# Performance work log

Hardware: AMD Instinct MI355X
Metric: run time of the kernel (lower is better)

The kernel has to match this reference:

```python
import jax, jax.numpy as jnp
import numpy as np

B = 512          # batch
D = 2048         # num_variables / leaf folds of a balanced binary region graph
K = 32           # num_units (sum/input units per fold)


def setup_inputs() -> dict:
    key = jax.random.key(0)
    k1, k2, k3 = jax.random.split(key, 3)
    # input-layer log-densities per (variable-region, unit): [B, D, K]
    x = jax.random.normal(k1, (B, D, K), dtype=jnp.float32)
    # packed per-fold CP mixing weights for all inner layers: sum_l F_l = D-1 folds
    weights = jax.random.uniform(k2, (D - 1, K, K), dtype=jnp.float32,
                                 minval=0.01, maxval=1.0)  # positive (monotonic)
    # packed fold_idx bookkeeping: layer l gathers children (2f, 2f+1) of prev layer
    idx_list = []
    F = D
    while F > 1:
        F //= 2
        idx_list.append(np.arange(2 * F, dtype=np.int32).reshape(F, 2))
    fold_idx = jnp.asarray(np.concatenate(idx_list, axis=0))  # [D-1, 2]
    # out-mixture logits over the root's K units (num_classes = 1)
    mix_logw = jax.random.normal(k3, (K,), dtype=jnp.float32)
    return {"x": x, "weights": weights, "fold_idx": fold_idx, "mix_logw": mix_logw}


def _log_matmul_exp(a, w):
    # a: [B, F, K] log-values; w: [F, K, Kout] positive weights
    # y_j = log sum_i exp(a_i) * w_ij, computed stably via max-subtraction
    m = jnp.max(a, axis=-1, keepdims=True)
    y = jnp.einsum('bfi,fij->bfj', jnp.exp(a - m), w)
    return jnp.log(y) + m


def reference(x, weights, fold_idx, mix_logw):
    # DAG evaluation: gather via fold_idx, CP layer = log-product of the two
    # gathered children followed by a per-fold log-linear mixture.
    out = x                      # [B, F, K]
    off = 0
    F = x.shape[1]
    while F > 1:                 # static Python loop over log2(D)=11 layers
        F //= 2
        idx = fold_idx[off:off + F]            # [F, 2] child indices (static slice)
        inp = out[:, idx, :]                   # gather -> [B, F, 2, K]
        prod = inp[:, :, 0, :] + inp[:, :, 1, :]   # log-space product node
        out = _log_matmul_exp(prod, weights[off:off + F])  # sum node -> [B, F, K]
        off += F
    # Born real path: outputs = 2 * real(log amp), then MonotonicMixtureLayer
    flat = 2.0 * out[:, 0, :]                  # [B, K]
    logw = jax.nn.log_softmax(mix_logw)        # normalized mixture weights
    return jax.nn.logsumexp(flat + logw[None, :], axis=-1)  # [B]
```

## Files before the change

kernel.cpp:

```cpp
#include <hip/hip_runtime.h>

#define KK 32
#define BATCH 512
#define DD 2048
#define ESTRIDE 36
#define NUNIT (KK * BATCH)

__device__ __forceinline__ float max8(const float p[8]) {
  const float a0 = fmaxf(p[0], p[1]), a1 = fmaxf(p[2], p[3]);
  const float a2 = fmaxf(p[4], p[5]), a3 = fmaxf(p[6], p[7]);
  return fmaxf(fmaxf(a0, a1), fmaxf(a2, a3));
}
__device__ __forceinline__ float max4pm(const float* pm, int lane) {
  return fmaxf(fmaxf(pm[lane], pm[65 + lane]),
               fmaxf(pm[130 + lane], pm[195 + lane]));
}
__device__ __forceinline__ void write_e(float* __restrict__ E, int lane,
                                        int j0, const float p[8], float m) {
  float4* ew = reinterpret_cast<float4*>(E + lane * ESTRIDE + j0);
  ew[0] = make_float4(__expf(p[0] - m), __expf(p[1] - m), __expf(p[2] - m),
                      __expf(p[3] - m));
  ew[1] = make_float4(__expf(p[4] - m), __expf(p[5] - m), __expf(p[6] - m),
                      __expf(p[7] - m));
}
__device__ __forceinline__ void addv8(const float a[8], const float b[8],
                                      float o[8]) {
#pragma unroll
  for (int j = 0; j < 8; ++j) o[j] = a[j] + b[j];
}

#define MAC8(acc, e, w0, w1)                                   \
  acc[0] = fmaf(e, w0.x, acc[0]); acc[1] = fmaf(e, w0.y, acc[1]); \
  acc[2] = fmaf(e, w0.z, acc[2]); acc[3] = fmaf(e, w0.w, acc[3]); \
  acc[4] = fmaf(e, w1.x, acc[4]); acc[5] = fmaf(e, w1.y, acc[5]); \
  acc[6] = fmaf(e, w1.z, acc[6]); acc[7] = fmaf(e, w1.w, acc[7]);

__device__ __forceinline__ void node8_pair(
    const float pa[8], const float pb[8], const float* __restrict__ Wa,
    const float* __restrict__ Wb, float* __restrict__ Ea,
    float* __restrict__ Eb, float* __restrict__ pm, int jg, int lane, int j0,
    float oa[8], float ob[8]) {
  pm[jg * 65 + lane] = max8(pa);
  pm[260 + jg * 65 + lane] = max8(pb);
  __syncthreads();
  const float ma = max4pm(pm, lane);
  const float mb = max4pm(pm + 260, lane);
  write_e(Ea, lane, j0, pa, ma);
  write_e(Eb, lane, j0, pb, mb);
  __syncthreads();

  const float4* era = reinterpret_cast<const float4*>(Ea + lane * ESTRIDE);
  const float4* erb = reinterpret_cast<const float4*>(Eb + lane * ESTRIDE);
  const float4* WLa = reinterpret_cast<const float4*>(Wa) + (j0 >> 2);
  const float4* WLb = reinterpret_cast<const float4*>(Wb) + (j0 >> 2);

  float acca[8], accb[8];
#pragma unroll
  for (int j = 0; j < 8; ++j) { acca[j] = 0.0f; accb[j] = 0.0f; }

#pragma unroll 1
  for (int q = 0; q < 8; ++q) {
    const float4 eva = era[q];
    const float4 evb = erb[q];
    const int i0 = 4 * q;
    {
      const float4 w0 = WLa[(i0 + 0) * 8], w1 = WLa[(i0 + 0) * 8 + 1];
      const float4 v0 = WLb[(i0 + 0) * 8], v1 = WLb[(i0 + 0) * 8 + 1];
      MAC8(acca, eva.x, w0, w1) MAC8(accb, evb.x, v0, v1)
    }
    {
      const float4 w0 = WLa[(i0 + 1) * 8], w1 = WLa[(i0 + 1) * 8 + 1];
      const float4 v0 = WLb[(i0 + 1) * 8], v1 = WLb[(i0 + 1) * 8 + 1];
      MAC8(acca, eva.y, w0, w1) MAC8(accb, evb.y, v0, v1)
    }
    {
      const float4 w0 = WLa[(i0 + 2) * 8], w1 = WLa[(i0 + 2) * 8 + 1];
      const float4 v0 = WLb[(i0 + 2) * 8], v1 = WLb[(i0 + 2) * 8 + 1];
      MAC8(acca, eva.z, w0, w1) MAC8(accb, evb.z, v0, v1)
    }
    {
      const float4 w0 = WLa[(i0 + 3) * 8], w1 = WLa[(i0 + 3) * 8 + 1];
      const float4 v0 = WLb[(i0 + 3) * 8], v1 = WLb[(i0 + 3) * 8 + 1];
      MAC8(acca, eva.w, w0, w1) MAC8(accb, evb.w, v0, v1)
    }
  }
#pragma unroll
  for (int j = 0; j < 8; ++j) {
    oa[j] = __logf(acca[j]) + ma;
    ob[j] = __logf(accb[j]) + mb;
  }
}

__device__ __forceinline__ void node8L(const float p8[8],
                                       const float* __restrict__ Wt,
                                       float* __restrict__ E,
                                       float* __restrict__ pm, int jg,
                                       int lane, int j0, float o8[8]) {
  pm[jg * 65 + lane] = max8(p8);
  __syncthreads();
  const float m = max4pm(pm, lane);
  write_e(E, lane, j0, p8, m);
  __syncthreads();

  const float4* er = reinterpret_cast<const float4*>(E + lane * ESTRIDE);
  const float4* WL = reinterpret_cast<const float4*>(Wt) + (j0 >> 2);
  float acc[8];
#pragma unroll
  for (int j = 0; j < 8; ++j) acc[j] = 0.0f;
#pragma unroll 1
  for (int q = 0; q < 8; ++q) {
    const float4 ev = er[q];
    const int i0 = 4 * q;
    const float4 wa0 = WL[(i0 + 0) * 8], wa1 = WL[(i0 + 0) * 8 + 1];
    const float4 wb0 = WL[(i0 + 1) * 8], wb1 = WL[(i0 + 1) * 8 + 1];
    const float4 wc0 = WL[(i0 + 2) * 8], wc1 = WL[(i0 + 2) * 8 + 1];
    const float4 wd0 = WL[(i0 + 3) * 8], wd1 = WL[(i0 + 3) * 8 + 1];
    MAC8(acc, ev.x, wa0, wa1) MAC8(acc, ev.y, wb0, wb1)
    MAC8(acc, ev.z, wc0, wc1) MAC8(acc, ev.w, wd0, wd1)
  }
#pragma unroll
  for (int j = 0; j < 8; ++j) o8[j] = __logf(acc[j]) + m;
}

__device__ __forceinline__ void pairload_x(const float* __restrict__ xb,
                                           int leaf, int j0, float p[8]) {
  const float4* u = reinterpret_cast<const float4*>(xb + leaf * KK + j0);
  const float4* v = reinterpret_cast<const float4*>(xb + (leaf + 1) * KK + j0);
  const float4 u0 = u[0], u1 = u[1], v0 = v[0], v1 = v[1];
  p[0] = u0.x + v0.x; p[1] = u0.y + v0.y; p[2] = u0.z + v0.z; p[3] = u0.w + v0.w;
  p[4] = u1.x + v1.x; p[5] = u1.y + v1.y; p[6] = u1.z + v1.z; p[7] = u1.w + v1.w;
}

__device__ __forceinline__ void pairload_n(const float* __restrict__ in,
                                           int node, int j0, int b, float p[8]) {
  const float* p0 = in + (size_t)node * NUNIT + (size_t)j0 * BATCH + b;
  const float* p1 = p0 + NUNIT;
#pragma unroll
  for (int k = 0; k < 8; ++k) p[k] = p0[k * BATCH] + p1[k * BATCH];
}

__global__ __launch_bounds__(256, 4) void kern1(const float* __restrict__ x,
                                                const float* __restrict__ W,
                                                float* __restrict__ o) {
  __shared__ __align__(16) float W_lds[7 * KK * KK];
  __shared__ __align__(16) float Ea[64 * ESTRIDE];
  __shared__ __align__(16) float Eb[64 * ESTRIDE];
  __shared__ float pm[2 * 260];
  const int tid = threadIdx.x;
  const int lane = tid & 63;
  const int jg = __builtin_amdgcn_readfirstlane(tid >> 6);
  const int j0 = jg * 8;
  const int b = blockIdx.y * 64 + lane;
  const int chunk = blockIdx.x;
  const int c4 = chunk * 4, c2 = chunk * 2;

  const float4* W4 = reinterpret_cast<const float4*>(W);
  float4* WL4 = reinterpret_cast<float4*>(W_lds);
  WL4[tid]        = W4[(size_t)(c4 + 0) * 256 + tid];
  WL4[256 + tid]  = W4[(size_t)(c4 + 1) * 256 + tid];
  WL4[512 + tid]  = W4[(size_t)(c4 + 2) * 256 + tid];
  WL4[768 + tid]  = W4[(size_t)(c4 + 3) * 256 + tid];
  WL4[1024 + tid] = W4[(size_t)(1024 + c2 + 0) * 256 + tid];
  WL4[1280 + tid] = W4[(size_t)(1024 + c2 + 1) * 256 + tid];
  WL4[1536 + tid] = W4[(size_t)(1536 + chunk) * 256 + tid];

  const float* xb = x + (size_t)b * (DD * KK) + (size_t)chunk * 8 * KK;
  float pA0[8], pB0[8], pA1[8], pB1[8];
  pairload_x(xb, 0, j0, pA0);
  pairload_x(xb, 2, j0, pB0);
  pairload_x(xb, 4, j0, pA1);
  pairload_x(xb, 6, j0, pB1);

  float n0[8], n1[8], n2[8], n3[8], m0[8], m1[8], o8[8], p[8], q[8];

  node8_pair(pA0, pB0, W_lds + 0 * 1024, W_lds + 1 * 1024, Ea, Eb, pm, jg,
             lane, j0, n0, n1);
  node8_pair(pA1, pB1, W_lds + 2 * 1024, W_lds + 3 * 1024, Ea, Eb, pm, jg,
             lane, j0, n2, n3);
  addv8(n0, n1, p);
  addv8(n2, n3, q);
  node8_pair(p, q, W_lds + 4 * 1024, W_lds + 5 * 1024, Ea, Eb, pm, jg, lane,
             j0, m0, m1);
  addv8(m0, m1, p);
  node8L(p, W_lds + 6 * 1024, Ea, pm, jg, lane, j0, o8);

#pragma unroll
  for (int j = 0; j < 8; ++j)
    o[(size_t)chunk * NUNIT + (size_t)(j0 + j) * BATCH + b] = o8[j];
}

__global__ __launch_bounds__(256, 4) void kernT(const float* __restrict__ in,
                                                const float* __restrict__ W,
                                                float* __restrict__ o, int lo,
                                                int hi) {
  __shared__ __align__(16) float W_lds[3 * KK * KK];
  __shared__ __align__(16) float Ea[64 * ESTRIDE];
  __shared__ __align__(16) float Eb[64 * ESTRIDE];
  __shared__ float pm[2 * 260];
  const int tid = threadIdx.x;
  const int lane = tid & 63;
  const int jg = __builtin_amdgcn_readfirstlane(tid >> 6);
  const int j0 = jg * 8;
  const int b = blockIdx.y * 64 + lane;
  const int n = blockIdx.x;

  const float4* W4 = reinterpret_cast<const float4*>(W);
  float4* WL4 = reinterpret_cast<float4*>(W_lds);
  WL4[tid]       = W4[(size_t)(lo + 2 * n + 0) * 256 + tid];
  WL4[256 + tid] = W4[(size_t)(lo + 2 * n + 1) * 256 + tid];
  WL4[512 + tid] = W4[(size_t)(hi + n) * 256 + tid];

  float pa[8], pb[8], r0[8], r1[8], p[8], o8[8];
  pairload_n(in, 4 * n + 0, j0, b, pa);
  pairload_n(in, 4 * n + 2, j0, b, pb);
  node8_pair(pa, pb, W_lds, W_lds + 1024, Ea, Eb, pm, jg, lane, j0, r0, r1);
  addv8(r0, r1, p);
  node8L(p, W_lds + 2048, Ea, pm, jg, lane, j0, o8);

#pragma unroll
  for (int j = 0; j < 8; ++j)
    o[(size_t)n * NUNIT + (size_t)(j0 + j) * BATCH + b] = o8[j];
}

__global__ __launch_bounds__(256, 4) void kernF(const float* __restrict__ in,
                                                const float* __restrict__ W,
                                                const float* __restrict__ mixw,
                                                float* __restrict__ out) {
  __shared__ __align__(16) float W_lds[3 * KK * KK];
  __shared__ __align__(16) float Ea[64 * ESTRIDE];
  __shared__ __align__(16) float Eb[64 * ESTRIDE];
  __shared__ float pm[2 * 260];
  const int tid = threadIdx.x;
  const int lane = tid & 63;
  const int jg = __builtin_amdgcn_readfirstlane(tid >> 6);
  const int j0 = jg * 8;
  const int b = blockIdx.y * 64 + lane;

  const float4* W4 = reinterpret_cast<const float4*>(W);
  float4* WL4 = reinterpret_cast<float4*>(W_lds);
  WL4[tid]       = W4[(size_t)2044 * 256 + tid];
  WL4[256 + tid] = W4[(size_t)2045 * 256 + tid];
  WL4[512 + tid] = W4[(size_t)2046 * 256 + tid];

  float pa[8], pb[8], r0[8], r1[8], p[8], o8[8];
  pairload_n(in, 0, j0, b, pa);
  pairload_n(in, 2, j0, b, pb);
  node8_pair(pa, pb, W_lds, W_lds + 1024, Ea, Eb, pm, jg, lane, j0, r0, r1);
  addv8(r0, r1, p);
  node8L(p, W_lds + 2048, Ea, pm, jg, lane, j0, o8);

  float wv32[KK];
#pragma unroll
  for (int i = 0; i < KK; ++i) wv32[i] = mixw[i];
  float t[KK];
#pragma unroll
  for (int i = 0; i < KK; ++i) t[i] = wv32[i];
#pragma unroll
  for (int s = KK / 2; s >= 1; s >>= 1)
#pragma unroll
    for (int i = 0; i < s; ++i) t[i] = fmaxf(t[i], t[i + s]);
  const float wm = t[0];
  float ws = 0.0f;
#pragma unroll
  for (int i = 0; i < KK; ++i) ws += __expf(wv32[i] - wm);
  const float lsew = __logf(ws) + wm;

  float t8[8];
#pragma unroll
  for (int j = 0; j < 8; ++j) t8[j] = 2.0f * o8[j] + (wv32[j0 + j] - lsew);
  __syncthreads();
  pm[jg * 65 + lane] = max8(t8);
  __syncthreads();
  const float m2 = max4pm(pm, lane);
  float ss = 0.0f;
#pragma unroll
  for (int j = 0; j < 8; ++j) ss += __expf(t8[j] - m2);
  __syncthreads();
  pm[jg * 65 + lane] = ss;
  __syncthreads();
  if (jg == 0) {
    const float s4 = (pm[lane] + pm[65 + lane]) + (pm[130 + lane] + pm[195 + lane]);
    out[b] = __logf(s4) + m2;
  }
}

extern "C" void kernel_launch(void* const* d_in, const int* in_sizes, int n_in,
                              void* d_out, int out_size, void* d_ws,
                              size_t ws_size, hipStream_t stream) {
  const float* x = (const float*)d_in[0];
  const float* W = (const float*)d_in[1];
  const float* mixw = (const float*)d_in[3];
  float* out = (float*)d_out;

  float* A = (float*)d_ws;
  float* Bb = A + (size_t)256 * NUNIT;

  kern1<<<dim3(256, 8), 256, 0, stream>>>(x, W, A);
  kernT<<<dim3(64, 8), 256, 0, stream>>>(A, W, Bb, 1792, 1920);
  kernT<<<dim3(16, 8), 256, 0, stream>>>(Bb, W, A, 1984, 2016);
  kernT<<<dim3(4, 8), 256, 0, stream>>>(A, W, Bb, 2032, 2040);
  kernF<<<dim3(1, 8), 256, 0, stream>>>(Bb, W, mixw, out);
}
```

Before: 244.0 us.

## Compute full 32-unit nodes per thread in registers, drop LDS and barriers

Each thread now owns one batch element and evaluates whole 32-wide nodes in registers. Weights are read directly from global memory at block-uniform addresses, so they can be served by scalar loads, and the LDS staging plus the cross-wave max reductions and their barriers are gone. Intermediate activations switch from a unit-major [node][unit][batch] layout to [node][batch][unit], so each thread reads and writes its own contiguous rows with float4 accesses. The trade-off is much higher register pressure (several 32-float arrays live at once) and four times fewer launched blocks, which lowers occupancy and leaves less room to hide latency.

```diff
diff --git a/kernel.cpp b/kernel.cpp
--- a/kernel.cpp
+++ b/kernel.cpp
@@ -3,285 +3,181 @@
 #define KK 32
 #define BATCH 512
 #define DD 2048
-#define ESTRIDE 36
-#define NUNIT (KK * BATCH)
+#define NODEF (BATCH * KK)
 
-__device__ __forceinline__ float max8(const float p[8]) {
-  const float a0 = fmaxf(p[0], p[1]), a1 = fmaxf(p[2], p[3]);
-  const float a2 = fmaxf(p[4], p[5]), a3 = fmaxf(p[6], p[7]);
-  return fmaxf(fmaxf(a0, a1), fmaxf(a2, a3));
-}
-__device__ __forceinline__ float max4pm(const float* pm, int lane) {
-  return fmaxf(fmaxf(pm[lane], pm[65 + lane]),
-               fmaxf(pm[130 + lane], pm[195 + lane]));
-}
-__device__ __forceinline__ void write_e(float* __restrict__ E, int lane,
-                                        int j0, const float p[8], float m) {
-  float4* ew = reinterpret_cast<float4*>(E + lane * ESTRIDE + j0);
-  ew[0] = make_float4(__expf(p[0] - m), __expf(p[1] - m), __expf(p[2] - m),
-                      __expf(p[3] - m));
-  ew[1] = make_float4(__expf(p[4] - m), __expf(p[5] - m), __expf(p[6] - m),
-                      __expf(p[7] - m));
-}
-__device__ __forceinline__ void addv8(const float a[8], const float b[8],
-                                      float o[8]) {
+__device__ __forceinline__ void node32(float p[KK], const float* __restrict__ Wn) {
+  float t[16];
 #pragma unroll
-  for (int j = 0; j < 8; ++j) o[j] = a[j] + b[j];
+  for (int i = 0; i < 16; ++i) t[i] = fmaxf(p[2 * i], p[2 * i + 1]);
+#pragma unroll
+  for (int s = 8; s >= 1; s >>= 1)
+#pragma unroll
+    for (int i = 0; i < s; ++i) t[i] = fmaxf(t[i], t[i + s]);
+  const float m = t[0];
+
+#pragma unroll
+  for (int i = 0; i < KK; ++i) p[i] = __expf(p[i] - m);
+
+  float acc[KK];
+#pragma unroll
+  for (int j = 0; j < KK; ++j) acc[j] = 0.0f;
+
+#pragma unroll 8
+  for (int i = 0; i < KK; ++i) {
+    const float ei = p[i];
+#pragma unroll
+    for (int j = 0; j < KK; ++j)
+      acc[j] = fmaf(ei, Wn[i * KK + j], acc[j]);
+  }
+
+#pragma unroll
+  for (int j = 0; j < KK; ++j) p[j] = __logf(acc[j]) + m;
 }
 
-#define MAC8(acc, e, w0, w1)                                   \
-  acc[0] = fmaf(e, w0.x, acc[0]); acc[1] = fmaf(e, w0.y, acc[1]); \
-  acc[2] = fmaf(e, w0.z, acc[2]); acc[3] = fmaf(e, w0.w, acc[3]); \
-  acc[4] = fmaf(e, w1.x, acc[4]); acc[5] = fmaf(e, w1.y, acc[5]); \
-  acc[6] = fmaf(e, w1.z, acc[6]); acc[7] = fmaf(e, w1.w, acc[7]);
-
-__device__ __forceinline__ void node8_pair(
-    const float pa[8], const float pb[8], const float* __restrict__ Wa,
-    const float* __restrict__ Wb, float* __restrict__ Ea,
-    float* __restrict__ Eb, float* __restrict__ pm, int jg, int lane, int j0,
-    float oa[8], float ob[8]) {
-  pm[jg * 65 + lane] = max8(pa);
-  pm[260 + jg * 65 + lane] = max8(pb);
-  __syncthreads();
-  const float ma = max4pm(pm, lane);
-  const float mb = max4pm(pm + 260, lane);
-  write_e(Ea, lane, j0, pa, ma);
-  write_e(Eb, lane, j0, pb, mb);
-  __syncthreads();
-
-  const float4* era = reinterpret_cast<const float4*>(Ea + lane * ESTRIDE);
-  const float4* erb = reinterpret_cast<const float4*>(Eb + lane * ESTRIDE);
-  const float4* WLa = reinterpret_cast<const float4*>(Wa) + (j0 >> 2);
-  const float4* WLb = reinterpret_cast<const float4*>(Wb) + (j0 >> 2);
-
-  float acca[8], accb[8];
+__device__ __forceinline__ void pairsum_g(const float* __restrict__ a,
+                                          const float* __restrict__ b,
+                                          float p[KK]) {
+  const float4* u = reinterpret_cast<const float4*>(a);
+  const float4* v = reinterpret_cast<const float4*>(b);
+  float4 ub[8], vb[8];
 #pragma unroll
-  for (int j = 0; j < 8; ++j) { acca[j] = 0.0f; accb[j] = 0.0f; }
-
-#pragma unroll 1
+  for (int q = 0; q < 8; ++q) ub[q] = u[q];
+#pragma unroll
+  for (int q = 0; q < 8; ++q) vb[q] = v[q];
+#pragma unroll
   for (int q = 0; q < 8; ++q) {
-    const float4 eva = era[q];
-    const float4 evb = erb[q];
-    const int i0 = 4 * q;
-    {
-      const float4 w0 = WLa[(i0 + 0) * 8], w1 = WLa[(i0 + 0) * 8 + 1];
-      const float4 v0 = WLb[(i0 + 0) * 8], v1 = WLb[(i0 + 0) * 8 + 1];
-      MAC8(acca, eva.x, w0, w1) MAC8(accb, evb.x, v0, v1)
-    }
-    {
-      const float4 w0 = WLa[(i0 + 1) * 8], w1 = WLa[(i0 + 1) * 8 + 1];
-      const float4 v0 = WLb[(i0 + 1) * 8], v1 = WLb[(i0 + 1) * 8 + 1];
-      MAC8(acca, eva.y, w0, w1) MAC8(accb, evb.y, v0, v1)
-    }
-    {
-      const float4 w0 = WLa[(i0 + 2) * 8], w1 = WLa[(i0 + 2) * 8 + 1];
-      const float4 v0 = WLb[(i0 + 2) * 8], v1 = WLb[(i0 + 2) * 8 + 1];
-      MAC8(acca, eva.z, w0, w1) MAC8(accb, evb.z, v0, v1)
-    }
-    {
-      const float4 w0 = WLa[(i0 + 3) * 8], w1 = WLa[(i0 + 3) * 8 + 1];
-      const float4 v0 = WLb[(i0 + 3) * 8], v1 = WLb[(i0 + 3) * 8 + 1];
-      MAC8(acca, eva.w, w0, w1) MAC8(accb, evb.w, v0, v1)
-    }
-  }
-#pragma unroll
-  for (int j = 0; j < 8; ++j) {
-    oa[j] = __logf(acca[j]) + ma;
-    ob[j] = __logf(accb[j]) + mb;
+    p[4 * q + 0] = ub[q].x + vb[q].x;
+    p[4 * q + 1] = ub[q].y + vb[q].y;
+    p[4 * q + 2] = ub[q].z + vb[q].z;
+    p[4 * q + 3] = ub[q].w + vb[q].w;
   }
 }
 
-__device__ __forceinline__ void node8L(const float p8[8],
-                                       const float* __restrict__ Wt,
-                                       float* __restrict__ E,
-                                       float* __restrict__ pm, int jg,
-                                       int lane, int j0, float o8[8]) {
-  pm[jg * 65 + lane] = max8(p8);
-  __syncthreads();
-  const float m = max4pm(pm, lane);
-  write_e(E, lane, j0, p8, m);
-  __syncthreads();
-
-  const float4* er = reinterpret_cast<const float4*>(E + lane * ESTRIDE);
-  const float4* WL = reinterpret_cast<const float4*>(Wt) + (j0 >> 2);
-  float acc[8];
+__device__ __forceinline__ void store32(float* __restrict__ dst, const float p[KK]) {
+  float4* d = reinterpret_cast<float4*>(dst);
 #pragma unroll
-  for (int j = 0; j < 8; ++j) acc[j] = 0.0f;
-#pragma unroll 1
-  for (int q = 0; q < 8; ++q) {
-    const float4 ev = er[q];
-    const int i0 = 4 * q;
-    const float4 wa0 = WL[(i0 + 0) * 8], wa1 = WL[(i0 + 0) * 8 + 1];
-    const float4 wb0 = WL[(i0 + 1) * 8], wb1 = WL[(i0 + 1) * 8 + 1];
-    const float4 wc0 = WL[(i0 + 2) * 8], wc1 = WL[(i0 + 2) * 8 + 1];
-    const float4 wd0 = WL[(i0 + 3) * 8], wd1 = WL[(i0 + 3) * 8 + 1];
-    MAC8(acc, ev.x, wa0, wa1) MAC8(acc, ev.y, wb0, wb1)
-    MAC8(acc, ev.z, wc0, wc1) MAC8(acc, ev.w, wd0, wd1)
-  }
-#pragma unroll
-  for (int j = 0; j < 8; ++j) o8[j] = __logf(acc[j]) + m;
+  for (int q = 0; q < 8; ++q)
+    d[q] = make_float4(p[4 * q], p[4 * q + 1], p[4 * q + 2], p[4 * q + 3]);
 }
 
-__device__ __forceinline__ void pairload_x(const float* __restrict__ xb,
-                                           int leaf, int j0, float p[8]) {
-  const float4* u = reinterpret_cast<const float4*>(xb + leaf * KK + j0);
-  const float4* v = reinterpret_cast<const float4*>(xb + (leaf + 1) * KK + j0);
-  const float4 u0 = u[0], u1 = u[1], v0 = v[0], v1 = v[1];
-  p[0] = u0.x + v0.x; p[1] = u0.y + v0.y; p[2] = u0.z + v0.z; p[3] = u0.w + v0.w;
-  p[4] = u1.x + v1.x; p[5] = u1.y + v1.y; p[6] = u1.z + v1.z; p[7] = u1.w + v1.w;
+__global__ __launch_bounds__(256) void kern1(const float* __restrict__ x,
+                                             const float* __restrict__ W,
+                                             float* __restrict__ o) {
+  const int tid = threadIdx.x;
+  const int lane = tid & 63;
+  const int wid = tid >> 6;
+  const int chunk = blockIdx.x;
+  const int b = blockIdx.y * 256 + wid * 64 + lane;
+
+  const float* xb = x + (size_t)b * (DD * KK) + (size_t)chunk * 8 * KK;
+  const float* WL1 = W + (size_t)(4 * chunk) * (KK * KK);
+  const float* WL2 = W + (size_t)(1024 + 2 * chunk) * (KK * KK);
+  const float* WL3 = W + (size_t)(1536 + chunk) * (KK * KK);
+
+  float s01[KK], s23[KK], p[KK];
+
+  pairsum_g(xb + 0 * KK, xb + 1 * KK, s01);
+  node32(s01, WL1 + 0 * 1024);
+  pairsum_g(xb + 2 * KK, xb + 3 * KK, p);
+  node32(p, WL1 + 1 * 1024);
+#pragma unroll
+  for (int j = 0; j < KK; ++j) s01[j] += p[j];
+
+  pairsum_g(xb + 4 * KK, xb + 5 * KK, s23);
+  node32(s23, WL1 + 2 * 1024);
+  pairsum_g(xb + 6 * KK, xb + 7 * KK, p);
+  node32(p, WL1 + 3 * 1024);
+#pragma unroll
+  for (int j = 0; j < KK; ++j) s23[j] += p[j];
+
+  node32(s01, WL2 + 0 * 1024);
+  node32(s23, WL2 + 1 * 1024);
+#pragma unroll
+  for (int j = 0; j < KK; ++j) s01[j] += s23[j];
+
+  node32(s01, WL3);
+
+  store32(o + ((size_t)chunk * BATCH + b) * KK, s01);
 }
 
-__device__ __forceinline__ void pairload_n(const float* __restrict__ in,
-                                           int node, int j0, int b, float p[8]) {
-  const float* p0 = in + (size_t)node * NUNIT + (size_t)j0 * BATCH + b;
-  const float* p1 = p0 + NUNIT;
+__global__ __launch_bounds__(256) void kernT(const float* __restrict__ in,
+                                             const float* __restrict__ W,
+                                             float* __restrict__ o, int lo,
+                                             int hi) {
+  const int tid = threadIdx.x;
+  const int lane = tid & 63;
+  const int wid = tid >> 6;
+  const int n = blockIdx.x;
+  const int b = blockIdx.y * 256 + wid * 64 + lane;
+
+  const float* i0 = in + ((size_t)(4 * n) * BATCH + b) * KK;
+
+  float s01[KK], p[KK];
+
+  pairsum_g(i0, i0 + NODEF, s01);
+  node32(s01, W + (size_t)(lo + 2 * n + 0) * (KK * KK));
+  pairsum_g(i0 + 2 * (size_t)NODEF, i0 + 3 * (size_t)NODEF, p);
+  node32(p, W + (size_t)(lo + 2 * n + 1) * (KK * KK));
 #pragma unroll
-  for (int k = 0; k < 8; ++k) p[k] = p0[k * BATCH] + p1[k * BATCH];
+  for (int j = 0; j < KK; ++j) s01[j] += p[j];
+
+  node32(s01, W + (size_t)(hi + n) * (KK * KK));
+
+  store32(o + ((size_t)n * BATCH + b) * KK, s01);
 }
 
-__global__ __launch_bounds__(256, 4) void kern1(const float* __restrict__ x,
-                                                const float* __restrict__ W,
-                                                float* __restrict__ o) {
-  __shared__ __align__(16) float W_lds[7 * KK * KK];
-  __shared__ __align__(16) float Ea[64 * ESTRIDE];
-  __shared__ __align__(16) float Eb[64 * ESTRIDE];
-  __shared__ float pm[2 * 260];
+__global__ __launch_bounds__(256) void kernF(const float* __restrict__ in,
+                                             const float* __restrict__ W,
+                                             const float* __restrict__ mixw,
+                                             float* __restrict__ out) {
   const int tid = threadIdx.x;
   const int lane = tid & 63;
-  const int jg = __builtin_amdgcn_readfirstlane(tid >> 6);
-  const int j0 = jg * 8;
-  const int b = blockIdx.y * 64 + lane;
-  const int chunk = blockIdx.x;
-  const int c4 = chunk * 4, c2 = chunk * 2;
+  const int wid = tid >> 6;
+  const int b = blockIdx.y * 256 + wid * 64 + lane;
 
-  const float4* W4 = reinterpret_cast<const float4*>(W);
-  float4* WL4 = reinterpret_cast<float4*>(W_lds);
-  WL4[tid]        = W4[(size_t)(c4 + 0) * 256 + tid];
-  WL4[256 + tid]  = W4[(size_t)(c4 + 1) * 256 + tid];
-  WL4[512 + tid]  = W4[(size_t)(c4 + 2) * 256 + tid];
-  WL4[768 + tid]  = W4[(size_t)(c4 + 3) * 256 + tid];
-  WL4[1024 + tid] = W4[(size_t)(1024 + c2 + 0) * 256 + tid];
-  WL4[1280 + tid] = W4[(size_t)(1024 + c2 + 1) * 256 + tid];
-  WL4[1536 + tid] = W4[(size_t)(1536 + chunk) * 256 + tid];
+  const float* i0 = in + (size_t)b * KK;
 
-  const float* xb = x + (size_t)b * (DD * KK) + (size_t)chunk * 8 * KK;
-  float pA0[8], pB0[8], pA1[8], pB1[8];
-  pairload_x(xb, 0, j0, pA0);
-  pairload_x(xb, 2, j0, pB0);
-  pairload_x(xb, 4, j0, pA1);
-  pairload_x(xb, 6, j0, pB1);
+  float s01[KK], p[KK];
 
-  float n0[8], n1[8], n2[8], n3[8], m0[8], m1[8], o8[8], p[8], q[8];
+  pairsum_g(i0, i0 + NODEF, s01);
+  node32(s01, W + (size_t)2044 * (KK * KK));
+  pairsum_g(i0 + 2 * (size_t)NODEF, i0 + 3 * (size_t)NODEF, p);
+  node32(p, W + (size_t)2045 * (KK * KK));
+#pragma unroll
+  for (int j = 0; j < KK; ++j) s01[j] += p[j];
 
-  node8_pair(pA0, pB0, W_lds + 0 * 1024, W_lds + 1 * 1024, Ea, Eb, pm, jg,
-             lane, j0, n0, n1);
-  node8_pair(pA1, pB1, W_lds + 2 * 1024, W_lds + 3 * 1024, Ea, Eb, pm, jg,
-             lane, j0, n2, n3);
-  addv8(n0, n1, p);
-  addv8(n2, n3, q);
-  node8_pair(p, q, W_lds + 4 * 1024, W_lds + 5 * 1024, Ea, Eb, pm, jg, lane,
-             j0, m0, m1);
-  addv8(m0, m1, p);
-  node8L(p, W_lds + 6 * 1024, Ea, pm, jg, lane, j0, o8);
+  node32(s01, W + (size_t)2046 * (KK * KK));
 
+  float wv[KK];
 #pragma unroll
-  for (int j = 0; j < 8; ++j)
-    o[(size_t)chunk * NUNIT + (size_t)(j0 + j) * BATCH + b] = o8[j];
-}
-
-__global__ __launch_bounds__(256, 4) void kernT(const float* __restrict__ in,
-                                                const float* __restrict__ W,
-                                                float* __restrict__ o, int lo,
-                                                int hi) {
-  __shared__ __align__(16) float W_lds[3 * KK * KK];
-  __shared__ __align__(16) float Ea[64 * ESTRIDE];
-  __shared__ __align__(16) float Eb[64 * ESTRIDE];
-  __shared__ float pm[2 * 260];
-  const int tid = threadIdx.x;
-  const int lane = tid & 63;
-  const int jg = __builtin_amdgcn_readfirstlane(tid >> 6);
-  const int j0 = jg * 8;
-  const int b = blockIdx.y * 64 + lane;
-  const int n = blockIdx.x;
-
-  const float4* W4 = reinterpret_cast<const float4*>(W);
-  float4* WL4 = reinterpret_cast<float4*>(W_lds);
-  WL4[tid]       = W4[(size_t)(lo + 2 * n + 0) * 256 + tid];
-  WL4[256 + tid] = W4[(size_t)(lo + 2 * n + 1) * 256 + tid];
-  WL4[512 + tid] = W4[(size_t)(hi + n) * 256 + tid];
-
-  float pa[8], pb[8], r0[8], r1[8], p[8], o8[8];
-  pairload_n(in, 4 * n + 0, j0, b, pa);
-  pairload_n(in, 4 * n + 2, j0, b, pb);
-  node8_pair(pa, pb, W_lds, W_lds + 1024, Ea, Eb, pm, jg, lane, j0, r0, r1);
-  addv8(r0, r1, p);
-  node8L(p, W_lds + 2048, Ea, pm, jg, lane, j0, o8);
-
+  for (int i = 0; i < KK; ++i) wv[i] = mixw[i];
+  float t[16];
 #pragma unroll
-  for (int j = 0; j < 8; ++j)
-    o[(size_t)n * NUNIT + (size_t)(j0 + j) * BATCH + b] = o8[j];
-}
-
-__global__ __launch_bounds__(256, 4) void kernF(const float* __restrict__ in,
-                                                const float* __restrict__ W,
-                                                const float* __restrict__ mixw,
-                                                float* __restrict__ out) {
-  __shared__ __align__(16) float W_lds[3 * KK * KK];
-  __shared__ __align__(16) float Ea[64 * ESTRIDE];
-  __shared__ __align__(16) float Eb[64 * ESTRIDE];
-  __shared__ float pm[2 * 260];
-  const int tid = threadIdx.x;
-  const int lane = tid & 63;
-  const int jg = __builtin_amdgcn_readfirstlane(tid >> 6);
-  const int j0 = jg * 8;
-  const int b = blockIdx.y * 64 + lane;
-
-  const float4* W4 = reinterpret_cast<const float4*>(W);
-  float4* WL4 = reinterpret_cast<float4*>(W_lds);
-  WL4[tid]       = W4[(size_t)2044 * 256 + tid];
-  WL4[256 + tid] = W4[(size_t)2045 * 256 + tid];
-  WL4[512 + tid] = W4[(size_t)2046 * 256 + tid];
-
-  float pa[8], pb[8], r0[8], r1[8], p[8], o8[8];
-  pairload_n(in, 0, j0, b, pa);
-  pairload_n(in, 2, j0, b, pb);
-  node8_pair(pa, pb, W_lds, W_lds + 1024, Ea, Eb, pm, jg, lane, j0, r0, r1);
-  addv8(r0, r1, p);
-  node8L(p, W_lds + 2048, Ea, pm, jg, lane, j0, o8);
-
-  float wv32[KK];
+  for (int i = 0; i < 16; ++i) t[i] = fmaxf(wv[2 * i], wv[2 * i + 1]);
 #pragma unroll
-  for (int i = 0; i < KK; ++i) wv32[i] = mixw[i];
-  float t[KK];
-#pragma unroll
-  for (int i = 0; i < KK; ++i) t[i] = wv32[i];
-#pragma unroll
-  for (int s = KK / 2; s >= 1; s >>= 1)
+  for (int s = 8; s >= 1; s >>= 1)
 #pragma unroll
     for (int i = 0; i < s; ++i) t[i] = fmaxf(t[i], t[i + s]);
   const float wm = t[0];
   float ws = 0.0f;
 #pragma unroll
-  for (int i = 0; i < KK; ++i) ws += __expf(wv32[i] - wm);
+  for (int i = 0; i < KK; ++i) ws += __expf(wv[i] - wm);
   const float lsew = __logf(ws) + wm;
 
-  float t8[8];
+  float f[KK];
 #pragma unroll
-  for (int j = 0; j < 8; ++j) t8[j] = 2.0f * o8[j] + (wv32[j0 + j] - lsew);
-  __syncthreads();
-  pm[jg * 65 + lane] = max8(t8);
-  __syncthreads();
-  const float m2 = max4pm(pm, lane);
+  for (int j = 0; j < KK; ++j) f[j] = 2.0f * s01[j] + (wv[j] - lsew);
+#pragma unroll
+  for (int i = 0; i < 16; ++i) t[i] = fmaxf(f[2 * i], f[2 * i + 1]);
+#pragma unroll
+  for (int s = 8; s >= 1; s >>= 1)
+#pragma unroll
+    for (int i = 0; i < s; ++i) t[i] = fmaxf(t[i], t[i + s]);
+  const float m2 = t[0];
   float ss = 0.0f;
 #pragma unroll
-  for (int j = 0; j < 8; ++j) ss += __expf(t8[j] - m2);
-  __syncthreads();
-  pm[jg * 65 + lane] = ss;
-  __syncthreads();
-  if (jg == 0) {
-    const float s4 = (pm[lane] + pm[65 + lane]) + (pm[130 + lane] + pm[195 + lane]);
-    out[b] = __logf(s4) + m2;
-  }
+  for (int j = 0; j < KK; ++j) ss += __expf(f[j] - m2);
+  out[b] = __logf(ss) + m2;
 }
 
 extern "C" void kernel_launch(void* const* d_in, const int* in_sizes, int n_in,
@@ -293,11 +189,11 @@
   float* out = (float*)d_out;
 
   float* A = (float*)d_ws;
-  float* Bb = A + (size_t)256 * NUNIT;
+  float* Bb = A + (size_t)256 * NODEF;
 
-  kern1<<<dim3(256, 8), 256, 0, stream>>>(x, W, A);
-  kernT<<<dim3(64, 8), 256, 0, stream>>>(A, W, Bb, 1792, 1920);
-  kernT<<<dim3(16, 8), 256, 0, stream>>>(Bb, W, A, 1984, 2016);
-  kernT<<<dim3(4, 8), 256, 0, stream>>>(A, W, Bb, 2032, 2040);
-  kernF<<<dim3(1, 8), 256, 0, stream>>>(Bb, W, mixw, out);
+  kern1<<<dim3(256, 2), 256, 0, stream>>>(x, W, A);
+  kernT<<<dim3(64, 2), 256, 0, stream>>>(A, W, Bb, 1792, 1920);
+  kernT<<<dim3(16, 2), 256, 0, stream>>>(Bb, W, A, 1984, 2016);
+  kernT<<<dim3(4, 2), 256, 0, stream>>>(A, W, Bb, 2032, 2040);
+  kernF<<<dim3(1, 2), 256, 0, stream>>>(Bb, W, mixw, out);
 }
```

Result: slower. 377.6 us (+54.7%).

## Reuse weight LDS slots across tree levels in kern1 to shrink shared memory

Applied to the files above, without the earlier changes.

Shrinks kern1's weight LDS buffer from seven to four 32x32 matrices. Weights for the upper levels are held in registers and written into freed LDS slots between the barriers of earlier node-pair stages. Less LDS per block should allow more resident blocks per CU and better latency hiding. The cost is extra registers held across stages, plus reliance on the existing barrier placement to avoid overwriting slots still being read.

```diff
diff --git a/kernel.cpp b/kernel.cpp
--- a/kernel.cpp
+++ b/kernel.cpp
@@ -35,11 +35,13 @@
   acc[4] = fmaf(e, w1.x, acc[4]); acc[5] = fmaf(e, w1.y, acc[5]); \
   acc[6] = fmaf(e, w1.z, acc[6]); acc[7] = fmaf(e, w1.w, acc[7]);
 
-__device__ __forceinline__ void node8_pair(
+template <int NST>
+__device__ __forceinline__ void node8_pairT(
     const float pa[8], const float pb[8], const float* __restrict__ Wa,
     const float* __restrict__ Wb, float* __restrict__ Ea,
     float* __restrict__ Eb, float* __restrict__ pm, int jg, int lane, int j0,
-    float oa[8], float ob[8]) {
+    float oa[8], float ob[8], int tid, float4* __restrict__ rdst, float4 rva,
+    float4 rvb) {
   pm[jg * 65 + lane] = max8(pa);
   pm[260 + jg * 65 + lane] = max8(pb);
   __syncthreads();
@@ -47,6 +49,8 @@
   const float mb = max4pm(pm + 260, lane);
   write_e(Ea, lane, j0, pa, ma);
   write_e(Eb, lane, j0, pb, mb);
+  if constexpr (NST >= 1) rdst[tid] = rva;
+  if constexpr (NST >= 2) rdst[256 + tid] = rvb;
   __syncthreads();
 
   const float4* era = reinterpret_cast<const float4*>(Ea + lane * ESTRIDE);
@@ -142,7 +146,7 @@
 __global__ __launch_bounds__(256, 4) void kern1(const float* __restrict__ x,
                                                 const float* __restrict__ W,
                                                 float* __restrict__ o) {
-  __shared__ __align__(16) float W_lds[7 * KK * KK];
+  __shared__ __align__(16) float W_lds[4 * KK * KK];
   __shared__ __align__(16) float Ea[64 * ESTRIDE];
   __shared__ __align__(16) float Eb[64 * ESTRIDE];
   __shared__ float pm[2 * 260];
@@ -156,13 +160,13 @@
 
   const float4* W4 = reinterpret_cast<const float4*>(W);
   float4* WL4 = reinterpret_cast<float4*>(W_lds);
-  WL4[tid]        = W4[(size_t)(c4 + 0) * 256 + tid];
-  WL4[256 + tid]  = W4[(size_t)(c4 + 1) * 256 + tid];
-  WL4[512 + tid]  = W4[(size_t)(c4 + 2) * 256 + tid];
-  WL4[768 + tid]  = W4[(size_t)(c4 + 3) * 256 + tid];
-  WL4[1024 + tid] = W4[(size_t)(1024 + c2 + 0) * 256 + tid];
-  WL4[1280 + tid] = W4[(size_t)(1024 + c2 + 1) * 256 + tid];
-  WL4[1536 + tid] = W4[(size_t)(1536 + chunk) * 256 + tid];
+  WL4[tid]       = W4[(size_t)(c4 + 0) * 256 + tid];
+  WL4[256 + tid] = W4[(size_t)(c4 + 1) * 256 + tid];
+  WL4[512 + tid] = W4[(size_t)(c4 + 2) * 256 + tid];
+  WL4[768 + tid] = W4[(size_t)(c4 + 3) * 256 + tid];
+  const float4 wr4 = W4[(size_t)(1024 + c2 + 0) * 256 + tid];
+  const float4 wr5 = W4[(size_t)(1024 + c2 + 1) * 256 + tid];
+  const float4 wr6 = W4[(size_t)(1536 + chunk) * 256 + tid];
 
   const float* xb = x + (size_t)b * (DD * KK) + (size_t)chunk * 8 * KK;
   float pA0[8], pB0[8], pA1[8], pB1[8];
@@ -173,16 +177,16 @@
 
   float n0[8], n1[8], n2[8], n3[8], m0[8], m1[8], o8[8], p[8], q[8];
 
-  node8_pair(pA0, pB0, W_lds + 0 * 1024, W_lds + 1 * 1024, Ea, Eb, pm, jg,
-             lane, j0, n0, n1);
-  node8_pair(pA1, pB1, W_lds + 2 * 1024, W_lds + 3 * 1024, Ea, Eb, pm, jg,
-             lane, j0, n2, n3);
+  node8_pairT<0>(pA0, pB0, W_lds + 0 * 1024, W_lds + 1 * 1024, Ea, Eb, pm, jg,
+                 lane, j0, n0, n1, tid, nullptr, wr4, wr4);
+  node8_pairT<2>(pA1, pB1, W_lds + 2 * 1024, W_lds + 3 * 1024, Ea, Eb, pm, jg,
+                 lane, j0, n2, n3, tid, WL4, wr4, wr5);
   addv8(n0, n1, p);
   addv8(n2, n3, q);
-  node8_pair(p, q, W_lds + 4 * 1024, W_lds + 5 * 1024, Ea, Eb, pm, jg, lane,
-             j0, m0, m1);
+  node8_pairT<1>(p, q, W_lds + 0 * 1024, W_lds + 1 * 1024, Ea, Eb, pm, jg,
+                 lane, j0, m0, m1, tid, WL4 + 512, wr6, wr6);
   addv8(m0, m1, p);
-  node8L(p, W_lds + 6 * 1024, Ea, pm, jg, lane, j0, o8);
+  node8L(p, W_lds + 2 * 1024, Ea, pm, jg, lane, j0, o8);
 
 #pragma unroll
   for (int j = 0; j < 8; ++j)
@@ -213,7 +217,9 @@
   float pa[8], pb[8], r0[8], r1[8], p[8], o8[8];
   pairload_n(in, 4 * n + 0, j0, b, pa);
   pairload_n(in, 4 * n + 2, j0, b, pb);
-  node8_pair(pa, pb, W_lds, W_lds + 1024, Ea, Eb, pm, jg, lane, j0, r0, r1);
+  node8_pairT<0>(pa, pb, W_lds, W_lds + 1024, Ea, Eb, pm, jg, lane, j0, r0,
+                 r1, tid, nullptr, make_float4(0, 0, 0, 0),
+                 make_float4(0, 0, 0, 0));
   addv8(r0, r1, p);
   node8L(p, W_lds + 2048, Ea, pm, jg, lane, j0, o8);
 
@@ -245,7 +251,9 @@
   float pa[8], pb[8], r0[8], r1[8], p[8], o8[8];
   pairload_n(in, 0, j0, b, pa);
   pairload_n(in, 2, j0, b, pb);
-  node8_pair(pa, pb, W_lds, W_lds + 1024, Ea, Eb, pm, jg, lane, j0, r0, r1);
+  node8_pairT<0>(pa, pb, W_lds, W_lds + 1024, Ea, Eb, pm, jg, lane, j0, r0,
+                 r1, tid, nullptr, make_float4(0, 0, 0, 0),
+                 make_float4(0, 0, 0, 0));
   addv8(r0, r1, p);
   node8L(p, W_lds + 2048, Ea, pm, jg, lane, j0, o8);
 
```

New measurement: 246.8 us. About the same (+1.1%).

## Shrink first-stage LDS via double-buffered weights and fuse upper layers into 3-level kernels

Applied to the files above, without the earlier changes.

The first kernel now processes nodes one at a time with a single E buffer and a two-slot weight buffer in LDS. The next weight tile is prefetched into registers and stored between barriers, which cuts LDS use and raises the occupancy target to 8 blocks per CU. The later layers are regrouped from three 2-level launches into two 3-level launches using a generalized kernel, removing one launch and one intermediate round-trip. In exchange, the single-node path loses the pairwise ILP of the old two-node routine, and the 3-level kernel launches with fewer blocks for the mid layers.

```diff
diff --git a/kernel.cpp b/kernel.cpp
--- a/kernel.cpp
+++ b/kernel.cpp
@@ -34,6 +34,40 @@
   acc[2] = fmaf(e, w0.z, acc[2]); acc[3] = fmaf(e, w0.w, acc[3]); \
   acc[4] = fmaf(e, w1.x, acc[4]); acc[5] = fmaf(e, w1.y, acc[5]); \
   acc[6] = fmaf(e, w1.z, acc[6]); acc[7] = fmaf(e, w1.w, acc[7]);
+
+template <bool RST>
+__device__ __forceinline__ void node1s(const float p[8],
+                                       const float* __restrict__ Wt,
+                                       float* __restrict__ E,
+                                       float* __restrict__ pm, int jg,
+                                       int lane, int j0, float o8[8], int tid,
+                                       float4* __restrict__ rdst, float4 wreg) {
+  pm[jg * 65 + lane] = max8(p);
+  __syncthreads();
+  const float m = max4pm(pm, lane);
+  write_e(E, lane, j0, p, m);
+  if constexpr (RST) rdst[tid] = wreg;
+  __syncthreads();
+
+  const float4* er = reinterpret_cast<const float4*>(E + lane * ESTRIDE);
+  const float4* WL = reinterpret_cast<const float4*>(Wt) + (j0 >> 2);
+  float acc[8];
+#pragma unroll
+  for (int j = 0; j < 8; ++j) acc[j] = 0.0f;
+#pragma unroll 1
+  for (int q = 0; q < 8; ++q) {
+    const float4 ev = er[q];
+    const int i0 = 4 * q;
+    const float4 wa0 = WL[(i0 + 0) * 8], wa1 = WL[(i0 + 0) * 8 + 1];
+    const float4 wb0 = WL[(i0 + 1) * 8], wb1 = WL[(i0 + 1) * 8 + 1];
+    const float4 wc0 = WL[(i0 + 2) * 8], wc1 = WL[(i0 + 2) * 8 + 1];
+    const float4 wd0 = WL[(i0 + 3) * 8], wd1 = WL[(i0 + 3) * 8 + 1];
+    MAC8(acc, ev.x, wa0, wa1) MAC8(acc, ev.y, wb0, wb1)
+    MAC8(acc, ev.z, wc0, wc1) MAC8(acc, ev.w, wd0, wd1)
+  }
+#pragma unroll
+  for (int j = 0; j < 8; ++j) o8[j] = __logf(acc[j]) + m;
+}
 
 __device__ __forceinline__ void node8_pair(
     const float pa[8], const float pb[8], const float* __restrict__ Wa,
@@ -139,9 +173,59 @@
   for (int k = 0; k < 8; ++k) p[k] = p0[k * BATCH] + p1[k * BATCH];
 }
 
-__global__ __launch_bounds__(256, 4) void kern1(const float* __restrict__ x,
+__global__ __launch_bounds__(256, 8) void kern1(const float* __restrict__ x,
                                                 const float* __restrict__ W,
                                                 float* __restrict__ o) {
+  __shared__ __align__(16) float Wl[2 * KK * KK];
+  __shared__ __align__(16) float E[64 * ESTRIDE];
+  __shared__ float pm[260];
+  const int tid = threadIdx.x;
+  const int lane = tid & 63;
+  const int jg = __builtin_amdgcn_readfirstlane(tid >> 6);
+  const int j0 = jg * 8;
+  const int b = blockIdx.y * 64 + lane;
+  const int chunk = blockIdx.x;
+  const int c4 = chunk * 4, c2 = chunk * 2;
+
+  const float4* W4 = reinterpret_cast<const float4*>(W);
+  float4* WL4 = reinterpret_cast<float4*>(Wl);
+  WL4[tid]       = W4[(size_t)(c4 + 0) * 256 + tid];
+  WL4[256 + tid] = W4[(size_t)(c4 + 1) * 256 + tid];
+
+  const float* xb = x + (size_t)b * (DD * KK) + (size_t)chunk * 8 * KK;
+  float p0[8], p1[8], p2[8], p3[8];
+  pairload_x(xb, 0, j0, p0);
+  pairload_x(xb, 2, j0, p1);
+  pairload_x(xb, 4, j0, p2);
+  pairload_x(xb, 6, j0, p3);
+
+  float n0[8], n1[8], n2[8], n3[8], o8[8];
+
+  float4 w2 = W4[(size_t)(c4 + 2) * 256 + tid];
+  node1s<false>(p0, Wl, E, pm, jg, lane, j0, n0, tid, nullptr, w2);
+  float4 w3 = W4[(size_t)(c4 + 3) * 256 + tid];
+  node1s<true>(p1, Wl + 1024, E, pm, jg, lane, j0, n1, tid, WL4, w2);
+  float4 w4 = W4[(size_t)(1024 + c2 + 0) * 256 + tid];
+  addv8(n0, n1, p0);
+  node1s<true>(p2, Wl, E, pm, jg, lane, j0, n2, tid, WL4 + 256, w3);
+  float4 w5 = W4[(size_t)(1024 + c2 + 1) * 256 + tid];
+  node1s<true>(p3, Wl + 1024, E, pm, jg, lane, j0, n3, tid, WL4, w4);
+  float4 w6 = W4[(size_t)(1536 + chunk) * 256 + tid];
+  addv8(n2, n3, p1);
+  node1s<true>(p0, Wl, E, pm, jg, lane, j0, n0, tid, WL4 + 256, w5);
+  node1s<true>(p1, Wl + 1024, E, pm, jg, lane, j0, n1, tid, WL4, w6);
+  addv8(n0, n1, p0);
+  node1s<false>(p0, Wl, E, pm, jg, lane, j0, o8, tid, nullptr, w6);
+
+#pragma unroll
+  for (int j = 0; j < 8; ++j)
+    o[(size_t)chunk * NUNIT + (size_t)(j0 + j) * BATCH + b] = o8[j];
+}
+
+__global__ __launch_bounds__(256, 4) void kern3L(const float* __restrict__ in,
+                                                 const float* __restrict__ W,
+                                                 float* __restrict__ o, int b4,
+                                                 int b2, int b1) {
   __shared__ __align__(16) float W_lds[7 * KK * KK];
   __shared__ __align__(16) float Ea[64 * ESTRIDE];
   __shared__ __align__(16) float Eb[64 * ESTRIDE];
@@ -151,25 +235,23 @@
   const int jg = __builtin_amdgcn_readfirstlane(tid >> 6);
   const int j0 = jg * 8;
   const int b = blockIdx.y * 64 + lane;
-  const int chunk = blockIdx.x;
-  const int c4 = chunk * 4, c2 = chunk * 2;
+  const int u = blockIdx.x;
 
   const float4* W4 = reinterpret_cast<const float4*>(W);
   float4* WL4 = reinterpret_cast<float4*>(W_lds);
-  WL4[tid]        = W4[(size_t)(c4 + 0) * 256 + tid];
-  WL4[256 + tid]  = W4[(size_t)(c4 + 1) * 256 + tid];
-  WL4[512 + tid]  = W4[(size_t)(c4 + 2) * 256 + tid];
-  WL4[768 + tid]  = W4[(size_t)(c4 + 3) * 256 + tid];
-  WL4[1024 + tid] = W4[(size_t)(1024 + c2 + 0) * 256 + tid];
-  WL4[1280 + tid] = W4[(size_t)(1024 + c2 + 1) * 256 + tid];
-  WL4[1536 + tid] = W4[(size_t)(1536 + chunk) * 256 + tid];
-
-  const float* xb = x + (size_t)b * (DD * KK) + (size_t)chunk * 8 * KK;
+  WL4[tid]        = W4[(size_t)(b4 + 4 * u + 0) * 256 + tid];
+  WL4[256 + tid]  = W4[(size_t)(b4 + 4 * u + 1) * 256 + tid];
+  WL4[512 + tid]  = W4[(size_t)(b4 + 4 * u + 2) * 256 + tid];
+  WL4[768 + tid]  = W4[(size_t)(b4 + 4 * u + 3) * 256 + tid];
+  WL4[1024 + tid] = W4[(size_t)(b2 + 2 * u + 0) * 256 + tid];
+  WL4[1280 + tid] = W4[(size_t)(b2 + 2 * u + 1) * 256 + tid];
+  WL4[1536 + tid] = W4[(size_t)(b1 + u) * 256 + tid];
+
   float pA0[8], pB0[8], pA1[8], pB1[8];
-  pairload_x(xb, 0, j0, pA0);
-  pairload_x(xb, 2, j0, pB0);
-  pairload_x(xb, 4, j0, pA1);
-  pairload_x(xb, 6, j0, pB1);
+  pairload_n(in, 8 * u + 0, j0, b, pA0);
+  pairload_n(in, 8 * u + 2, j0, b, pB0);
+  pairload_n(in, 8 * u + 4, j0, b, pA1);
+  pairload_n(in, 8 * u + 6, j0, b, pB1);
 
   float n0[8], n1[8], n2[8], n3[8], m0[8], m1[8], o8[8], p[8], q[8];
 
@@ -186,40 +268,7 @@
 
 #pragma unroll
   for (int j = 0; j < 8; ++j)
-    o[(size_t)chunk * NUNIT + (size_t)(j0 + j) * BATCH + b] = o8[j];
-}
-
-__global__ __launch_bounds__(256, 4) void kernT(const float* __restrict__ in,
-                                                const float* __restrict__ W,
-                                                float* __restrict__ o, int lo,
-                                                int hi) {
-  __shared__ __align__(16) float W_lds[3 * KK * KK];
-  __shared__ __align__(16) float Ea[64 * ESTRIDE];
-  __shared__ __align__(16) float Eb[64 * ESTRIDE];
-  __shared__ float pm[2 * 260];
-  const int tid = threadIdx.x;
-  const int lane = tid & 63;
-  const int jg = __builtin_amdgcn_readfirstlane(tid >> 6);
-  const int j0 = jg * 8;
-  const int b = blockIdx.y * 64 + lane;
-  const int n = blockIdx.x;
-
-  const float4* W4 = reinterpret_cast<const float4*>(W);
-  float4* WL4 = reinterpret_cast<float4*>(W_lds);
-  WL4[tid]       = W4[(size_t)(lo + 2 * n + 0) * 256 + tid];
-  WL4[256 + tid] = W4[(size_t)(lo + 2 * n + 1) * 256 + tid];
-  WL4[512 + tid] = W4[(size_t)(hi + n) * 256 + tid];
-
-  float pa[8], pb[8], r0[8], r1[8], p[8], o8[8];
-  pairload_n(in, 4 * n + 0, j0, b, pa);
-  pairload_n(in, 4 * n + 2, j0, b, pb);
-  node8_pair(pa, pb, W_lds, W_lds + 1024, Ea, Eb, pm, jg, lane, j0, r0, r1);
-  addv8(r0, r1, p);
-  node8L(p, W_lds + 2048, Ea, pm, jg, lane, j0, o8);
-
-#pragma unroll
-  for (int j = 0; j < 8; ++j)
-    o[(size_t)n * NUNIT + (size_t)(j0 + j) * BATCH + b] = o8[j];
+    o[(size_t)u * NUNIT + (size_t)(j0 + j) * BATCH + b] = o8[j];
 }
 
 __global__ __launch_bounds__(256, 4) void kernF(const float* __restrict__ in,
@@ -294,10 +343,10 @@
 
   float* A = (float*)d_ws;
   float* Bb = A + (size_t)256 * NUNIT;
+  float* Cc = Bb + (size_t)32 * NUNIT;
 
   kern1<<<dim3(256, 8), 256, 0, stream>>>(x, W, A);
-  kernT<<<dim3(64, 8), 256, 0, stream>>>(A, W, Bb, 1792, 1920);
-  kernT<<<dim3(16, 8), 256, 0, stream>>>(Bb, W, A, 1984, 2016);
-  kernT<<<dim3(4, 8), 256, 0, stream>>>(A, W, Bb, 2032, 2040);
-  kernF<<<dim3(1, 8), 256, 0, stream>>>(Bb, W, mixw, out);
-}
+  kern3L<<<dim3(32, 8), 256, 0, stream>>>(A, W, Bb, 1792, 1920, 1984);
+  kern3L<<<dim3(4, 8), 256, 0, stream>>>(Bb, W, Cc, 2016, 2032, 2040);
+  kernF<<<dim3(1, 8), 256, 0, stream>>>(Cc, W, mixw, out);
+}
```

After: 285.8 us. +17.1%, slower.
